# Performance work log

Measured on AMD Instinct MI355X. Metric: run time of the kernel, lower is better.

## Reference

```python
import jax, jax.numpy as jnp
import numpy as np

N = 50000
E = 800000
NUM_GRAPHS = 128
X_IN, HID, EDGE_DIM = 64, 64, 16


def setup_inputs() -> dict:
    key = jax.random.key(0)
    ks = jax.random.split(key, 9)
    s = 0.05
    inp = {
        'x': jax.random.normal(ks[0], (N, X_IN), jnp.float32),
        'edge_index': jax.random.randint(ks[1], (2, E), 0, N, dtype=jnp.int32),
        'edge_attr': jax.random.normal(ks[2], (E, EDGE_DIM), jnp.float32),
        'batch': jnp.sort(jax.random.randint(ks[3], (N,), 0, NUM_GRAPHS, dtype=jnp.int32)),
        'w_fc1': jax.random.normal(ks[4], (EDGE_DIM, 1), jnp.float32) * s,
        'b_fc1': jnp.zeros((1,), jnp.float32),
    }
    dims = [(X_IN, HID), (HID, HID * 2), (HID * 2, HID)]
    for i, (din, dout) in enumerate(dims):
        k1, k2, k3 = jax.random.split(ks[5 + i], 3)
        inp[f'w1_{i}'] = jax.random.normal(k1, (din, dout), jnp.float32) * s
        inp[f'b1_{i}'] = jnp.zeros((dout,), jnp.float32)
        inp[f'w2_{i}'] = jax.random.normal(k2, (din, dout), jnp.float32) * s
        inp[f'w3_{i}'] = jax.random.normal(k3, (din, dout), jnp.float32) * s
        inp[f'b3_{i}'] = jnp.zeros((dout,), jnp.float32)
    return inp


def leconv(x, src, dst, ew, w1, b1, w2, w3, b3):
    # PyG LEConv: out_i = lin3(x_i) + sum_{j->i} e_ji * (lin1(x_j) - lin2(x_i))
    a = x @ w1 + b1          # lin1 (bias=True)   [N, out]
    b = x @ w2               # lin2 (bias=False)  [N, out]
    msg = ew[:, None] * (a[src] - b[dst])          # [E, out]
    agg = jax.ops.segment_sum(msg, dst, num_segments=N)
    return agg + x @ w3 + b3  # lin3 (bias=True)


def reference(x, edge_index, edge_attr, batch,
              w_fc1, b_fc1,
              w1_0, b1_0, w2_0, w3_0, b3_0,
              w1_1, b1_1, w2_1, w3_1, b3_1,
              w1_2, b1_2, w2_2, w3_2, b3_2):
    src, dst = edge_index[0], edge_index[1]
    ew = (edge_attr @ w_fc1 + b_fc1)[:, 0]         # fc1(edge_attr).squeeze(-1) -> [E]
    h = jax.nn.elu(leconv(x, src, dst, ew, w1_0, b1_0, w2_0, w3_0, b3_0))
    h = jax.nn.elu(leconv(h, src, dst, ew, w1_1, b1_1, w2_1, w3_1, b3_1))
    h = jax.nn.elu(leconv(h, src, dst, ew, w1_2, b1_2, w2_2, w3_2, b3_2))
    # global max pool over nodes of each graph -> [NUM_GRAPHS, HID]
    return jax.ops.segment_max(h, batch, num_segments=NUM_GRAPHS)
```

## Files before the change

### kernel.cpp

```cpp
#include <hip/hip_runtime.h>
#include <math.h>

#define N_NODES 50000
#define N_EDGES 800000
#define NUM_GRAPHS_ 128
#define SCAN_NB 98
#define NPASS 4
#define NODES_PER_PASS 12500
#define HCHUNKS 128
#define EDGES_PER_CHUNK 6250
#define HWORDS 12500
#define TS_BPH 196

typedef unsigned short u16;
typedef unsigned int u32;
typedef __attribute__((ext_vector_type(8))) short bf16x8;
typedef __attribute__((ext_vector_type(4))) float f32x4;

__device__ __forceinline__ float elu_f(float v) {
    return v > 0.f ? v : (__expf(v) - 1.f);
}
__device__ __forceinline__ u16 f2bf(float f) {
    u32 u = __float_as_uint(f);
    u += 0x7FFFu + ((u >> 16) & 1u);
    return (u16)(u >> 16);
}
__device__ __forceinline__ float bf2f(u16 h) {
    return __uint_as_float(((u32)h) << 16);
}
__device__ __forceinline__ void bfpair(u32 v, float& lo, float& hi) {
    lo = __uint_as_float(v << 16);
    hi = __uint_as_float(v & 0xFFFF0000u);
}
__device__ __forceinline__ u32 packbf(float lo, float hi) {
    return (u32)f2bf(lo) | ((u32)f2bf(hi) << 16);
}

__device__ __forceinline__ void gather_rows8(
    const int2* __restrict__ csr, const uint4* __restrict__ x4,
    int beg, int end, int eg, int cg,
    float* acc, float& WS) {
    float A[8], B[8];
#pragma unroll
    for (int j = 0; j < 8; j++) { A[j] = 0.f; B[j] = 0.f; }
    float ws0 = 0.f, ws1 = 0.f;
    int p = beg + eg;
    for (; p + 8 < end; p += 16) {
        int2 e0 = csr[p];
        int2 e1 = csr[p + 8];
        uint4 v0 = x4[(size_t)e0.x * 8 + cg];
        uint4 v1 = x4[(size_t)e1.x * 8 + cg];
        float w0 = __int_as_float(e0.y);
        float w1 = __int_as_float(e1.y);
        float f0, f1;
        bfpair(v0.x, f0, f1); A[0] += w0 * f0; A[1] += w0 * f1;
        bfpair(v0.y, f0, f1); A[2] += w0 * f0; A[3] += w0 * f1;
        bfpair(v0.z, f0, f1); A[4] += w0 * f0; A[5] += w0 * f1;
        bfpair(v0.w, f0, f1); A[6] += w0 * f0; A[7] += w0 * f1;
        ws0 += w0;
        bfpair(v1.x, f0, f1); B[0] += w1 * f0; B[1] += w1 * f1;
        bfpair(v1.y, f0, f1); B[2] += w1 * f0; B[3] += w1 * f1;
        bfpair(v1.z, f0, f1); B[4] += w1 * f0; B[5] += w1 * f1;
        bfpair(v1.w, f0, f1); B[6] += w1 * f0; B[7] += w1 * f1;
        ws1 += w1;
    }
    if (p < end) {
        int2 e0 = csr[p];
        uint4 v0 = x4[(size_t)e0.x * 8 + cg];
        float w0 = __int_as_float(e0.y);
        float f0, f1;
        bfpair(v0.x, f0, f1); A[0] += w0 * f0; A[1] += w0 * f1;
        bfpair(v0.y, f0, f1); A[2] += w0 * f0; A[3] += w0 * f1;
        bfpair(v0.z, f0, f1); A[4] += w0 * f0; A[5] += w0 * f1;
        bfpair(v0.w, f0, f1); A[6] += w0 * f0; A[7] += w0 * f1;
        ws0 += w0;
    }
#pragma unroll
    for (int j = 0; j < 8; j++) acc[j] = A[j] + B[j];
    WS = ws0 + ws1;
}

__global__ void prep_kernel(const float* __restrict__ edge_attr,
                            const float* __restrict__ w_fc1,
                            const float* __restrict__ b_fc1,
                            const int* __restrict__ edge_index,
                            float* __restrict__ ew,
                            u16* __restrict__ dst16,
                            const float* __restrict__ x, u16* __restrict__ xb,
                            const float* __restrict__ w3_0, const float* __restrict__ w1_0, const float* __restrict__ w2_0,
                            const float* __restrict__ w3_1, const float* __restrict__ w1_1, const float* __restrict__ w2_1,
                            const float* __restrict__ w3_2, const float* __restrict__ w1_2, const float* __restrict__ w2_2,
                            u16* __restrict__ bp0, u16* __restrict__ bp1, u16* __restrict__ bp2) {
    const int b = blockIdx.x;
    if (b < 3125) {
        const int e = b * 256 + threadIdx.x;
        const float4* ea = (const float4*)(edge_attr + (size_t)e * 16);
        const float4* wf = (const float4*)w_fc1;
        float acc = b_fc1[0];
#pragma unroll
        for (int i = 0; i < 4; i++) {
            float4 a = ea[i], w = wf[i];
            acc += a.x * w.x + a.y * w.y + a.z * w.z + a.w * w.w;
        }
        ew[e] = acc;
        dst16[e] = (u16)edge_index[N_EDGES + e];
    } else if (b < 6250) {
        const int g = (b - 3125) * 256 + threadIdx.x;
        float4 v = ((const float4*)x)[g];
        uint2 o;
        o.x = packbf(v.x, v.y);
        o.y = packbf(v.z, v.w);
        ((uint2*)xb)[g] = o;
    } else {
        const int t = (b - 6250) * 256 + threadIdx.x;
        u16 buf[8];
        if (t < 4608) {
            int DOUT, lid;
            const float *w3, *w1, *w2;
            u16* bp;
            if (t < 1536) { DOUT = 64;  lid = t;        w3 = w3_0; w1 = w1_0; w2 = w2_0; bp = bp0; }
            else          { DOUT = 128; lid = t - 1536; w3 = w3_1; w1 = w1_1; w2 = w2_1; bp = bp1; }
            const int NT = DOUT / 16;
            const int lane = lid & 63;
            const int fragid = lid >> 6;
            const int chunk = fragid / NT;
            const int ntile = fragid % NT;
            const int n = ntile * 16 + (lane & 15);
            const int kbase = chunk * 32 + (lane >> 4) * 8;
#pragma unroll
            for (int j = 0; j < 8; j++) {
                int k = kbase + j;
                int region = k / 64;
                int kk = k - region * 64;
                float v = (region == 0) ? w3[kk * DOUT + n]
                        : (region == 1) ? w1[kk * DOUT + n]
                                        : -w2[kk * DOUT + n];
                buf[j] = f2bf(v);
            }
            *(bf16x8*)(bp + ((size_t)lid << 3)) = *(bf16x8*)buf;
        } else if (t < 7680) {
            const int lid = t - 4608;
            const int NT = 12;
            const int lane = lid & 63;
            const int fragid = lid >> 6;
            const int chunk = fragid / NT;
            const int ntile = fragid % NT;
            const int n = ntile * 16 + (lane & 15);
            const int kbase = chunk * 32 + (lane >> 4) * 8;
#pragma unroll
            for (int j = 0; j < 8; j++) {
                int k = kbase + j;
                float v = (n < 64)  ? w3_2[k * 64 + n]
                        : (n < 128) ? -w2_2[k * 64 + (n - 64)]
                                    : w1_2[k * 64 + (n - 128)];
                buf[j] = f2bf(v);
            }
            *(bf16x8*)(bp2 + ((size_t)lid << 3)) = *(bf16x8*)buf;
        }
    }
}

__global__ __launch_bounds__(256) void deg_hist_kernel(const u16* __restrict__ dst16,
                                                       u32* __restrict__ partial) {
    __shared__ u32 bins[HWORDS];
    const int c = blockIdx.x >> 1;
    const int p = blockIdx.x & 1;
    const int t = threadIdx.x;
    for (int i = t; i < HWORDS; i += 256) bins[i] = 0;
    __syncthreads();
    const int base = c * EDGES_PER_CHUNK;
    const int nlo = p * 25000;
    for (int i = t; i < EDGES_PER_CHUNK; i += 256) {
        const int b = (int)dst16[base + i] - nlo;
        if ((unsigned)b < 25000u)
            atomicAdd(&bins[b >> 1], 1u << ((b & 1) * 16));
    }
    __syncthreads();
    u32* outp = partial + (size_t)blockIdx.x * HWORDS;
    for (int i = t; i < HWORDS; i += 256) outp[i] = bins[i];
}

__global__ __launch_bounds__(256) void scan_chunks_kernel(const u32* __restrict__ partial,
                                                          u32* __restrict__ prefpack,
                                                          u32* __restrict__ degpack) {
    __shared__ u32 qsums[4][64];
    const int t = threadIdx.x;
    const int p = (blockIdx.x >= TS_BPH) ? 1 : 0;
    const int wh0 = (blockIdx.x - p * TS_BPH) << 6;
    const int wl = t & 63;
    const int cq = t >> 6;
    const int wh = wh0 + wl;
    const bool ok = wh < HWORDS;

    u32 vals[32];
#pragma unroll
    for (int i = 0; i < 32; i++) {
        const int c = cq * 32 + i;
        vals[i] = ok ? partial[(size_t)((c << 1) + p) * HWORDS + wh] : 0u;
    }
    u32 s = 0;
#pragma unroll
    for (int i = 0; i < 32; i++) s += vals[i];
    qsums[cq][wl] = s;
    __syncthreads();
    u32 run = 0;
#pragma unroll
    for (int j = 0; j < 4; j++)
        if (j < cq) run += qsums[j][wl];

    if (ok) {
        const int g = p * HWORDS + wh;
#pragma unroll
        for (int i = 0; i < 32; i++) {
            const int c = cq * 32 + i;
            prefpack[(size_t)c * 25000 + g] = run;
            run += vals[i];
        }
        if (cq == 3) degpack[g] = run;
    }
}

__global__ __launch_bounds__(256) void scan1_kernel(const u32* __restrict__ degpack,
                                                    int* __restrict__ rowptr,
                                                    int* __restrict__ blk_sums) {
    __shared__ int sh[256];
    const int t = threadIdx.x;
    const int base = blockIdx.x * 512;
    const int i0 = base + 2 * t, i1 = i0 + 1;
    int d0 = 0, d1 = 0;
    if (i0 < N_NODES) {
        u32 v = degpack[i0 >> 1];
        d0 = (int)(v & 0xFFFFu);
        d1 = (int)(v >> 16);
    }
    const int pair = d0 + d1;
    int v = pair;
    sh[t] = v;
    __syncthreads();
#pragma unroll
    for (int off = 1; off < 256; off <<= 1) {
        int add = (t >= off) ? sh[t - off] : 0;
        __syncthreads();
        v += add;
        sh[t] = v;
        __syncthreads();
    }
    const int excl = v - pair;
    if (i0 < N_NODES) rowptr[i0] = excl;
    if (i1 < N_NODES) rowptr[i1] = excl + d0;
    if (t == 255) blk_sums[blockIdx.x] = v;
}

__global__ __launch_bounds__(128) void scan2_kernel(const int* __restrict__ blk_sums,
                                                    int* __restrict__ blk_offs,
                                                    int* __restrict__ rowptr) {
    __shared__ int sh[128];
    const int t = threadIdx.x;
    const int orig = (t < SCAN_NB) ? blk_sums[t] : 0;
    int v = orig;
    sh[t] = v;
    __syncthreads();
#pragma unroll
    for (int off = 1; off < 128; off <<= 1) {
        int add = (t >= off) ? sh[t - off] : 0;
        __syncthreads();
        v += add;
        sh[t] = v;
        __syncthreads();
    }
    if (t < SCAN_NB) blk_offs[t] = v - orig;
    if (t == 127) rowptr[N_NODES] = v;
}

__global__ void scan3_kernel(int* __restrict__ rowptr,
                             const int* __restrict__ blk_offs) {
    int i = blockIdx.x * blockDim.x + threadIdx.x;
    if (i >= N_NODES) return;
    rowptr[i] += blk_offs[i >> 9];
}

__global__ __launch_bounds__(256) void place_kernel(const int* __restrict__ edge_index,
                                                    const float* __restrict__ ew,
                                                    const u16* __restrict__ dst16,
                                                    const int* __restrict__ rowptr,
                                                    const u32* __restrict__ prefpack,
                                                    int2* __restrict__ csr) {
    __shared__ int lcur[NODES_PER_PASS];
    const int pass = blockIdx.x & (NPASS - 1);
    const int c = blockIdx.x >> 2;
    const int lo = pass * NODES_PER_PASS;
    const int t = threadIdx.x;
    for (int i = t; i < NODES_PER_PASS; i += 256) lcur[i] = 0;
    __syncthreads();
    const int base = c * EDGES_PER_CHUNK;
    for (int i = t; i < EDGES_PER_CHUNK; i += 256) {
        const int e = base + i;
        const int d = (int)dst16[e];
        const int dl = d - lo;
        if ((unsigned)dl < (unsigned)NODES_PER_PASS) {
            u32 pw = prefpack[(size_t)c * 25000 + (d >> 1)];
            int pref = (int)((pw >> ((d & 1) * 16)) & 0xFFFFu);
            int lpos = atomicAdd(&lcur[dl], 1);
            int2 ent;
            ent.x = edge_index[e];
            ent.y = __float_as_int(ew[e]);
            csr[rowptr[d] + pref + lpos] = ent;
        }
    }
}

__global__ __launch_bounds__(1024) void fused_l0(
    const u16* __restrict__ xb, const int* __restrict__ rowptr,
    const int2* __restrict__ csr, const u16* __restrict__ Bp0,
    const float* __restrict__ bias1, const float* __restrict__ bias3,
    float* __restrict__ cvec, u16* __restrict__ h1out) {
    __shared__ u16 A[64][200];
    __shared__ float csh[64];
    const int tid = threadIdx.x;
    const int wv = tid >> 6;
    const int lane = tid & 63;
    const int node_base = blockIdx.x * 64;
    const uint4* x4 = (const uint4*)xb;
    const int cg = lane & 7;
    const int eg = lane >> 3;

    for (int k = 0; k < 4; k++) {
        const int row = wv * 4 + k;
        const int node = node_base + row;
        float sv[8];
#pragma unroll
        for (int j = 0; j < 8; j++) sv[j] = 0.f;
        float wsum = 0.f;
        if (node < N_NODES)
            gather_rows8(csr, x4, rowptr[node], rowptr[node + 1], eg, cg, sv, wsum);
#pragma unroll
        for (int off = 32; off >= 8; off >>= 1) {
#pragma unroll
            for (int j = 0; j < 8; j++) sv[j] += __shfl_xor(sv[j], off);
            wsum += __shfl_xor(wsum, off);
        }
        if (lane < 8) {
            const float cn = wsum;
            uint4 hv = {0u, 0u, 0u, 0u};
            if (node < N_NODES) hv = x4[(size_t)node * 8 + cg];
            uint4 so;
            so.x = packbf(sv[0], sv[1]);
            so.y = packbf(sv[2], sv[3]);
            so.z = packbf(sv[4], sv[5]);
            so.w = packbf(sv[6], sv[7]);
            *(uint4*)&A[row][cg * 8] = hv;
            *(uint4*)&A[row][64 + cg * 8] = so;
            float h0, h1f;
            uint4 co;
            bfpair(hv.x, h0, h1f); co.x = packbf(cn * h0, cn * h1f);
            bfpair(hv.y, h0, h1f); co.y = packbf(cn * h0, cn * h1f);
            bfpair(hv.z, h0, h1f); co.z = packbf(cn * h0, cn * h1f);
            bfpair(hv.w, h0, h1f); co.w = packbf(cn * h0, cn * h1f);
            *(uint4*)&A[row][128 + cg * 8] = co;
            if (cg == 0) {
                csh[row] = cn;
                if (node < N_NODES) cvec[node] = cn;
            }
        }
    }
    __syncthreads();

    const int l15 = lane & 15;
    const int q = lane >> 4;
    const int qo = q * 8;
    const int mt = wv >> 2, nt = wv & 3;
    f32x4 acc = {0.f, 0.f, 0.f, 0.f};
#pragma unroll
    for (int chunk = 0; chunk < 6; chunk++) {
        bf16x8 a = *(const bf16x8*)&A[mt * 16 + l15][chunk * 32 + qo];
        bf16x8 b = *(const bf16x8*)(Bp0 + (((size_t)(chunk * 4 + nt) * 64 + lane) << 3));
        acc = __builtin_amdgcn_mfma_f32_16x16x32_bf16(a, b, acc, 0, 0, 0);
    }
    const int col = nt * 16 + l15;
    const float B3 = bias3[col];
    const float B1 = bias1[col];
#pragma unroll
    for (int reg = 0; reg < 4; reg++) {
        const int lrow = mt * 16 + q * 4 + reg;
        const int row = node_base + lrow;
        if (row < N_NODES) {
            const float val = acc[reg] + B3 + csh[lrow] * B1;
            h1out[(size_t)row * 64 + col] = f2bf(elu_f(val));
        }
    }
}

__global__ __launch_bounds__(1024) void fused_l1(
    const u16* __restrict__ h1in, const int* __restrict__ rowptr,
    const int2* __restrict__ csr, const u16* __restrict__ Bp1,
    const u16* __restrict__ Bp2, const float* __restrict__ bias1,
    const float* __restrict__ bias3, u16* __restrict__ zu,
    u16* __restrict__ yb) {
    __shared__ u16 A[64][200];
    __shared__ u16 ht[64][136];
    __shared__ float csh[64];
    const int tid = threadIdx.x;
    const int wv = tid >> 6;
    const int lane = tid & 63;
    const int node_base = blockIdx.x * 64;
    const uint4* x4 = (const uint4*)h1in;
    const int cg = lane & 7;
    const int eg = lane >> 3;

    for (int k = 0; k < 4; k++) {
        const int row = wv * 4 + k;
        const int node = node_base + row;
        float sv[8];
#pragma unroll
        for (int j = 0; j < 8; j++) sv[j] = 0.f;
        float wsum = 0.f;
        if (node < N_NODES)
            gather_rows8(csr, x4, rowptr[node], rowptr[node + 1], eg, cg, sv, wsum);
#pragma unroll
        for (int off = 32; off >= 8; off >>= 1) {
#pragma unroll
            for (int j = 0; j < 8; j++) sv[j] += __shfl_xor(sv[j], off);
            wsum += __shfl_xor(wsum, off);
        }
        if (lane < 8) {
            const float cn = wsum;
            uint4 hv = {0u, 0u, 0u, 0u};
            if (node < N_NODES) hv = x4[(size_t)node * 8 + cg];
            uint4 so;
            so.x = packbf(sv[0], sv[1]);
            so.y = packbf(sv[2], sv[3]);
            so.z = packbf(sv[4], sv[5]);
            so.w = packbf(sv[6], sv[7]);
            *(uint4*)&A[row][cg * 8] = hv;
            *(uint4*)&A[row][64 + cg * 8] = so;
            float h0, h1f;
            uint4 co;
            bfpair(hv.x, h0, h1f); co.x = packbf(cn * h0, cn * h1f);
            bfpair(hv.y, h0, h1f); co.y = packbf(cn * h0, cn * h1f);
            bfpair(hv.z, h0, h1f); co.z = packbf(cn * h0, cn * h1f);
            bfpair(hv.w, h0, h1f); co.w = packbf(cn * h0, cn * h1f);
            *(uint4*)&A[row][128 + cg * 8] = co;
            if (cg == 0) csh[row] = cn;
        }
    }
    __syncthreads();

    const int l15 = lane & 15;
    const int q = lane >> 4;
    const int qo = q * 8;

    {
        const int mt = wv >> 2;
        const int nt0 = (wv & 3) * 2;
        f32x4 acc0 = {0.f, 0.f, 0.f, 0.f};
        f32x4 acc1 = {0.f, 0.f, 0.f, 0.f};
#pragma unroll
        for (int chunk = 0; chunk < 6; chunk++) {
            bf16x8 a = *(const bf16x8*)&A[mt * 16 + l15][chunk * 32 + qo];
            bf16x8 bf0 = *(const bf16x8*)(Bp1 + (((size_t)(chunk * 8 + nt0) * 64 + lane) << 3));
            bf16x8 bf1 = *(const bf16x8*)(Bp1 + (((size_t)(chunk * 8 + nt0 + 1) * 64 + lane) << 3));
            acc0 = __builtin_amdgcn_mfma_f32_16x16x32_bf16(a, bf0, acc0, 0, 0, 0);
            acc1 = __builtin_amdgcn_mfma_f32_16x16x32_bf16(a, bf1, acc1, 0, 0, 0);
        }
#pragma unroll
        for (int ni = 0; ni < 2; ni++) {
            const int col = (nt0 + ni) * 16 + l15;
            const float B3 = bias3[col];
            const float B1 = bias1[col];
            const f32x4 av = ni ? acc1 : acc0;
#pragma unroll
            for (int reg = 0; reg < 4; reg++) {
                const int lrow = mt * 16 + q * 4 + reg;
                ht[lrow][col] = f2bf(elu_f(av[reg] + B3 + csh[lrow] * B1));
            }
        }
    }
    __syncthreads();

    {
        const int mt = wv >> 2;
        const int ntb = (wv & 3) * 3;
        f32x4 acc[3] = {};
#pragma unroll
        for (int chunk = 0; chunk < 4; chunk++) {
            bf16x8 a = *(const bf16x8*)&ht[mt * 16 + l15][chunk * 32 + qo];
#pragma unroll
            for (int j = 0; j < 3; j++) {
                bf16x8 b = *(const bf16x8*)(Bp2 + (((size_t)(chunk * 12 + ntb + j) * 64 + lane) << 3));
                acc[j] = __builtin_amdgcn_mfma_f32_16x16x32_bf16(a, b, acc[j], 0, 0, 0);
            }
        }
#pragma unroll
        for (int j = 0; j < 3; j++) {
            const int col = (ntb + j) * 16 + l15;
#pragma unroll
            for (int reg = 0; reg < 4; reg++) {
                const int row = node_base + mt * 16 + q * 4 + reg;
                if (row < N_NODES) {
                    const u16 v = f2bf(acc[j][reg]);
                    if (col < 128) zu[(size_t)row * 128 + col] = v;
                    else           yb[(size_t)row * 64 + (col - 128)] = v;
                }
            }
        }
    }
}

__global__ __launch_bounds__(256) void gather2_kernel(
    const u16* __restrict__ zu, const u16* __restrict__ yb,
    const int* __restrict__ rowptr, const int2* __restrict__ csr,
    const float* __restrict__ c, const float* __restrict__ bias1,
    const float* __restrict__ bias3, u16* __restrict__ h3) {
    const int gid = blockIdx.x * 256 + threadIdx.x;
    const int node = gid >> 6;
    if (node >= N_NODES) return;
    const int lane = threadIdx.x & 63;
    const int cg = lane & 7;
    const int eg = lane >> 3;

    float sv[8];
#pragma unroll
    for (int j = 0; j < 8; j++) sv[j] = 0.f;
    float wdummy = 0.f;
    gather_rows8(csr, (const uint4*)yb, rowptr[node], rowptr[node + 1], eg, cg,
                 sv, wdummy);

#pragma unroll
    for (int off = 32; off >= 8; off >>= 1) {
#pragma unroll
        for (int j = 0; j < 8; j++) sv[j] += __shfl_xor(sv[j], off);
    }

    if (lane < 8) {
        const float cn = c[node];
        const u16* zr = zu + (size_t)node * 128;
        uint4 zv = ((const uint4*)zr)[cg];
        uint4 uv = ((const uint4*)(zr + 64))[cg];
        float z0, z1, z2, z3, z4, z5, z6, z7;
        float u0, u1, u2, u3, u4, u5, u6, u7;
        bfpair(zv.x, z0, z1); bfpair(zv.y, z2, z3);
        bfpair(zv.z, z4, z5); bfpair(zv.w, z6, z7);
        bfpair(uv.x, u0, u1); bfpair(uv.y, u2, u3);
        bfpair(uv.z, u4, u5); bfpair(uv.w, u6, u7);
        const float4 b3a = *(const float4*)(bias3 + cg * 8);
        const float4 b3b = *(const float4*)(bias3 + cg * 8 + 4);
        const float4 b1a = *(const float4*)(bias1 + cg * 8);
        const float4 b1b = *(const float4*)(bias1 + cg * 8 + 4);
        float o0 = elu_f(z0 + cn * u0 + sv[0] + b3a.x + cn * b1a.x);
        float o1 = elu_f(z1 + cn * u1 + sv[1] + b3a.y + cn * b1a.y);
        float o2 = elu_f(z2 + cn * u2 + sv[2] + b3a.z + cn * b1a.z);
        float o3 = elu_f(z3 + cn * u3 + sv[3] + b3a.w + cn * b1a.w);
        float o4 = elu_f(z4 + cn * u4 + sv[4] + b3b.x + cn * b1b.x);
        float o5 = elu_f(z5 + cn * u5 + sv[5] + b3b.y + cn * b1b.y);
        float o6 = elu_f(z6 + cn * u6 + sv[6] + b3b.z + cn * b1b.z);
        float o7 = elu_f(z7 + cn * u7 + sv[7] + b3b.w + cn * b1b.w);
        uint4 ov;
        ov.x = packbf(o0, o1);
        ov.y = packbf(o2, o3);
        ov.z = packbf(o4, o5);
        ov.w = packbf(o6, o7);
        ((uint4*)h3)[(size_t)node * 8 + cg] = ov;
    }
}

__global__ void pool_kernel(const u16* __restrict__ h,
                            const int* __restrict__ batch,
                            float* __restrict__ out) {
    const int g = blockIdx.x;
    const int tid = threadIdx.x;
    int lo = 0, hi = N_NODES;
    while (lo < hi) { int mid = (lo + hi) >> 1; if (batch[mid] < g) lo = mid + 1; else hi = mid; }
    const int beg = lo;
    lo = beg; hi = N_NODES;
    while (lo < hi) { int mid = (lo + hi) >> 1; if (batch[mid] < g + 1) lo = mid + 1; else hi = mid; }
    const int end = lo;

    __shared__ float red[256];
    const int col = tid & 63;
    const int rg = tid >> 6;
    float m = -3.0e38f;
    for (int r = beg + rg; r < end; r += 4) m = fmaxf(m, bf2f(h[(size_t)r * 64 + col]));
    red[tid] = m;
    __syncthreads();
    if (tid < 64) {
        m = fmaxf(fmaxf(red[tid], red[tid + 64]), fmaxf(red[tid + 128], red[tid + 192]));
        out[g * 64 + tid] = m;
    }
}

extern "C" void kernel_launch(void* const* d_in, const int* in_sizes, int n_in,
                              void* d_out, int out_size, void* d_ws, size_t ws_size,
                              hipStream_t stream) {
    const float* x = (const float*)d_in[0];
    const int* ei = (const int*)d_in[1];
    const float* ea = (const float*)d_in[2];
    const int* batch = (const int*)d_in[3];
    const float* wfc = (const float*)d_in[4];
    const float* bfc = (const float*)d_in[5];
    const float* w1_0 = (const float*)d_in[6];
    const float* b1_0 = (const float*)d_in[7];
    const float* w2_0 = (const float*)d_in[8];
    const float* w3_0 = (const float*)d_in[9];
    const float* b3_0 = (const float*)d_in[10];
    const float* w1_1 = (const float*)d_in[11];
    const float* b1_1 = (const float*)d_in[12];
    const float* w2_1 = (const float*)d_in[13];
    const float* w3_1 = (const float*)d_in[14];
    const float* b3_1 = (const float*)d_in[15];
    const float* w1_2 = (const float*)d_in[16];
    const float* b1_2 = (const float*)d_in[17];
    const float* w2_2 = (const float*)d_in[18];
    const float* w3_2 = (const float*)d_in[19];
    const float* b3_2 = (const float*)d_in[20];
    float* out = (float*)d_out;

    char* ws = (char*)d_ws;
    float* ew      = (float*)(ws);
    float* c       = (float*)(ws + 3200000);
    int*   rowptr  = (int*)  (ws + 3800000);
    int2*  csr     = (int2*) (ws + 4000128);
    u16*   xb      = (u16*)  (ws + 10400128);
    u32*   partial = (u32*)  (ws + 16800128);
    u16*   dst16   = (u16*)  (ws + 29600128);
    u32*   degpack = (u32*)  (ws + 31600128);
    u16*   h1      = (u16*)  (ws + 42400128);
    u16*   zu      = (u16*)  (ws + 48800128);
    u16*   yb      = (u16*)  (ws + 61600128);
    u16*   bp0     = (u16*)  (ws + 68000128);
    u16*   bp1     = (u16*)  (ws + 68024704);
    u16*   bp2     = (u16*)  (ws + 68073856);
    int* blk_sums  = (int*)  (ws + 68123008);
    int* blk_offs  = (int*)  (ws + 68123520);
    u32* prefpack = (u32*)zu;
    u16* h3 = xb;

    prep_kernel<<<6280, 256, 0, stream>>>(ea, wfc, bfc, ei, ew, dst16, x, xb,
                                          w3_0, w1_0, w2_0, w3_1, w1_1, w2_1,
                                          w3_2, w1_2, w2_2, bp0, bp1, bp2);
    deg_hist_kernel<<<HCHUNKS * 2, 256, 0, stream>>>(dst16, partial);
    scan_chunks_kernel<<<TS_BPH * 2, 256, 0, stream>>>(partial, prefpack, degpack);
    scan1_kernel<<<SCAN_NB, 256, 0, stream>>>(degpack, rowptr, blk_sums);
    scan2_kernel<<<1, 128, 0, stream>>>(blk_sums, blk_offs, rowptr);
    scan3_kernel<<<(N_NODES + 255) / 256, 256, 0, stream>>>(rowptr, blk_offs);
    place_kernel<<<HCHUNKS * NPASS, 256, 0, stream>>>(ei, ew, dst16, rowptr, prefpack, csr);

    const int RB = (N_NODES + 63) / 64;
    const int GBLK = (N_NODES * 64 + 255) / 256;

    fused_l0<<<RB, 1024, 0, stream>>>(xb, rowptr, csr, bp0, b1_0, b3_0, c, h1);

    fused_l1<<<RB, 1024, 0, stream>>>(h1, rowptr, csr, bp1, bp2, b1_1, b3_1, zu, yb);

    gather2_kernel<<<GBLK, 256, 0, stream>>>(zu, yb, rowptr, csr, c, b1_2, b3_2, h3);

    pool_kernel<<<NUM_GRAPHS_, 256, 0, stream>>>(h3, batch, out);
}
```

Baseline: 327.1 us.

## Use full-range packed 16-bit LDS bins in histogram and CSR placement

The degree histogram and the CSR placement kernels now cover all 50000 destination nodes in a single 100KB LDS array of packed 16-bit counters, one 1024-thread block per edge chunk. The histogram no longer splits into two node halves, and the placement no longer runs four passes that each re-read the chunk's edges. Placement takes each edge's local rank from the old value of a packed 16-bit atomic. This removes redundant reads of dst16 and half the launched blocks, but leaves only 128 large blocks with high LDS use per block, which may limit occupancy.

```diff
diff --git a/kernel.cpp b/kernel.cpp
--- a/kernel.cpp
+++ b/kernel.cpp
@@ -5,12 +5,10 @@
 #define N_EDGES 800000
 #define NUM_GRAPHS_ 128
 #define SCAN_NB 98
-#define NPASS 4
-#define NODES_PER_PASS 12500
 #define HCHUNKS 128
 #define EDGES_PER_CHUNK 6250
-#define HWORDS 12500
-#define TS_BPH 196
+#define HWORDS2 25000
+#define TS_B 391
 
 typedef unsigned short u16;
 typedef unsigned int u32;
@@ -160,24 +158,21 @@
     }
 }
 
-__global__ __launch_bounds__(256) void deg_hist_kernel(const u16* __restrict__ dst16,
-                                                       u32* __restrict__ partial) {
-    __shared__ u32 bins[HWORDS];
-    const int c = blockIdx.x >> 1;
-    const int p = blockIdx.x & 1;
+__global__ __launch_bounds__(1024) void deg_hist_kernel(const u16* __restrict__ dst16,
+                                                        u32* __restrict__ partial) {
+    __shared__ u32 bins[HWORDS2];
+    const int c = blockIdx.x;
     const int t = threadIdx.x;
-    for (int i = t; i < HWORDS; i += 256) bins[i] = 0;
+    for (int i = t; i < HWORDS2; i += 1024) bins[i] = 0;
     __syncthreads();
     const int base = c * EDGES_PER_CHUNK;
-    const int nlo = p * 25000;
-    for (int i = t; i < EDGES_PER_CHUNK; i += 256) {
-        const int b = (int)dst16[base + i] - nlo;
-        if ((unsigned)b < 25000u)
-            atomicAdd(&bins[b >> 1], 1u << ((b & 1) * 16));
-    }
-    __syncthreads();
-    u32* outp = partial + (size_t)blockIdx.x * HWORDS;
-    for (int i = t; i < HWORDS; i += 256) outp[i] = bins[i];
+    for (int i = t; i < EDGES_PER_CHUNK; i += 1024) {
+        const int d = (int)dst16[base + i];
+        atomicAdd(&bins[d >> 1], 1u << ((d & 1) * 16));
+    }
+    __syncthreads();
+    u32* outp = partial + (size_t)c * HWORDS2;
+    for (int i = t; i < HWORDS2; i += 1024) outp[i] = bins[i];
 }
 
 __global__ __launch_bounds__(256) void scan_chunks_kernel(const u32* __restrict__ partial,
@@ -185,18 +180,16 @@
                                                           u32* __restrict__ degpack) {
     __shared__ u32 qsums[4][64];
     const int t = threadIdx.x;
-    const int p = (blockIdx.x >= TS_BPH) ? 1 : 0;
-    const int wh0 = (blockIdx.x - p * TS_BPH) << 6;
     const int wl = t & 63;
     const int cq = t >> 6;
-    const int wh = wh0 + wl;
-    const bool ok = wh < HWORDS;
+    const int g = blockIdx.x * 64 + wl;
+    const bool ok = g < HWORDS2;
 
     u32 vals[32];
 #pragma unroll
     for (int i = 0; i < 32; i++) {
         const int c = cq * 32 + i;
-        vals[i] = ok ? partial[(size_t)((c << 1) + p) * HWORDS + wh] : 0u;
+        vals[i] = ok ? partial[(size_t)c * HWORDS2 + g] : 0u;
     }
     u32 s = 0;
 #pragma unroll
@@ -209,11 +202,10 @@
         if (j < cq) run += qsums[j][wl];
 
     if (ok) {
-        const int g = p * HWORDS + wh;
 #pragma unroll
         for (int i = 0; i < 32; i++) {
             const int c = cq * 32 + i;
-            prefpack[(size_t)c * 25000 + g] = run;
+            prefpack[(size_t)c * HWORDS2 + g] = run;
             run += vals[i];
         }
         if (cq == 3) degpack[g] = run;
@@ -279,33 +271,30 @@
     rowptr[i] += blk_offs[i >> 9];
 }
 
-__global__ __launch_bounds__(256) void place_kernel(const int* __restrict__ edge_index,
-                                                    const float* __restrict__ ew,
-                                                    const u16* __restrict__ dst16,
-                                                    const int* __restrict__ rowptr,
-                                                    const u32* __restrict__ prefpack,
-                                                    int2* __restrict__ csr) {
-    __shared__ int lcur[NODES_PER_PASS];
-    const int pass = blockIdx.x & (NPASS - 1);
-    const int c = blockIdx.x >> 2;
-    const int lo = pass * NODES_PER_PASS;
+__global__ __launch_bounds__(1024) void place_kernel(const int* __restrict__ edge_index,
+                                                     const float* __restrict__ ew,
+                                                     const u16* __restrict__ dst16,
+                                                     const int* __restrict__ rowptr,
+                                                     const u32* __restrict__ prefpack,
+                                                     int2* __restrict__ csr) {
+    __shared__ u32 lrank[HWORDS2];
+    const int c = blockIdx.x;
     const int t = threadIdx.x;
-    for (int i = t; i < NODES_PER_PASS; i += 256) lcur[i] = 0;
+    for (int i = t; i < HWORDS2; i += 1024) lrank[i] = 0;
     __syncthreads();
     const int base = c * EDGES_PER_CHUNK;
-    for (int i = t; i < EDGES_PER_CHUNK; i += 256) {
+    for (int i = t; i < EDGES_PER_CHUNK; i += 1024) {
         const int e = base + i;
         const int d = (int)dst16[e];
-        const int dl = d - lo;
-        if ((unsigned)dl < (unsigned)NODES_PER_PASS) {
-            u32 pw = prefpack[(size_t)c * 25000 + (d >> 1)];
-            int pref = (int)((pw >> ((d & 1) * 16)) & 0xFFFFu);
-            int lpos = atomicAdd(&lcur[dl], 1);
-            int2 ent;
-            ent.x = edge_index[e];
-            ent.y = __float_as_int(ew[e]);
-            csr[rowptr[d] + pref + lpos] = ent;
-        }
+        const int sh = (d & 1) * 16;
+        const u32 old = atomicAdd(&lrank[d >> 1], 1u << sh);
+        const int lpos = (int)((old >> sh) & 0xFFFFu);
+        const u32 pw = prefpack[(size_t)c * HWORDS2 + (d >> 1)];
+        const int pref = (int)((pw >> sh) & 0xFFFFu);
+        int2 ent;
+        ent.x = edge_index[e];
+        ent.y = __float_as_int(ew[e]);
+        csr[rowptr[d] + pref + lpos] = ent;
     }
 }
 
@@ -637,12 +626,12 @@
     prep_kernel<<<6280, 256, 0, stream>>>(ea, wfc, bfc, ei, ew, dst16, x, xb,
                                           w3_0, w1_0, w2_0, w3_1, w1_1, w2_1,
                                           w3_2, w1_2, w2_2, bp0, bp1, bp2);
-    deg_hist_kernel<<<HCHUNKS * 2, 256, 0, stream>>>(dst16, partial);
-    scan_chunks_kernel<<<TS_BPH * 2, 256, 0, stream>>>(partial, prefpack, degpack);
+    deg_hist_kernel<<<HCHUNKS, 1024, 0, stream>>>(dst16, partial);
+    scan_chunks_kernel<<<TS_B, 256, 0, stream>>>(partial, prefpack, degpack);
     scan1_kernel<<<SCAN_NB, 256, 0, stream>>>(degpack, rowptr, blk_sums);
     scan2_kernel<<<1, 128, 0, stream>>>(blk_sums, blk_offs, rowptr);
     scan3_kernel<<<(N_NODES + 255) / 256, 256, 0, stream>>>(rowptr, blk_offs);
-    place_kernel<<<HCHUNKS * NPASS, 256, 0, stream>>>(ei, ew, dst16, rowptr, prefpack, csr);
+    place_kernel<<<HCHUNKS, 1024, 0, stream>>>(ei, ew, dst16, rowptr, prefpack, csr);
 
     const int RB = (N_NODES + 63) / 64;
     const int GBLK = (N_NODES * 64 + 255) / 256;
```

New measurement: 334.5 us. +2.2%, slower.
